# Performance work log

Measured on AMD Instinct MI355X. Metric: run time of the kernel, lower is better.

The kernel has to match this reference:

```python
import jax, jax.numpy as jnp
import numpy as np

B, S, DIM, DA = 64, 4096, 256, 64
NEG = -1e30

def setup_inputs() -> dict:
    key = jax.random.key(0)
    k1, k2, k3, k4 = jax.random.split(key, 4)
    h = jax.random.normal(k1, (B, S, DIM), dtype=jnp.float32)
    mask = jax.random.randint(k2, (B, S), 0, 2).astype(jnp.bool_)
    # xavier_uniform with gain=1.414 as in the torch module
    lim_a = 1.414 * np.sqrt(6.0 / (DIM + DA))
    lim_b = 1.414 * np.sqrt(6.0 / (DA + 1))
    a = jax.random.uniform(k3, (DIM, DA), minval=-lim_a, maxval=lim_a, dtype=jnp.float32)
    b = jax.random.uniform(k4, (DA, 1), minval=-lim_b, maxval=lim_b, dtype=jnp.float32)
    return {"h": h, "mask": mask, "a": a, "b": b}

def reference(h, mask, a, b):
    # e: (B, S) additive-attention logits
    e = jnp.einsum('bsk,ko->bs', jnp.tanh(jnp.einsum('bsd,dk->bsk', h, a)), b)
    e = e + mask.astype(e.dtype) * NEG  # True == padding -> -1e30
    attn = jax.nn.softmax(e, axis=1)    # softmax over seq dim
    # weighted sum over seq: (B, DIM)
    return jnp.einsum('bs,bsd->bd', attn, h)
```

## Files before the change

kernel.cpp:

```cpp
#include <hip/hip_runtime.h>
#include <hip/hip_bf16.h>

#define B_      64
#define S_      4096
#define DIM_    256
#define DA_     64
#define NEG_    (-1e30f)
#define CHUNKS_ 16
#define ROWS_   256
#define TILES_  4
#define LDH_    264
#define PSTR_   258

typedef _Float16 half8 __attribute__((ext_vector_type(8)));
typedef float float4v __attribute__((ext_vector_type(4)));

__global__ __launch_bounds__(256) void prep_kernel(
    const float* __restrict__ a, const void* __restrict__ mask,
    _Float16* __restrict__ at_sw, int* __restrict__ flag)
{
    int idx = blockIdx.x * 256 + threadIdx.x;
    int j    = idx & 7;
    int lane = (idx >> 3) & 63;
    int kbnt = idx >> 9;
    int kb   = kbnt & 7;
    int nt   = kbnt >> 3;
    int d  = kb * 32 + (lane >> 4) * 8 + j;
    int kf = nt * 16 + (lane & 15);
    at_sw[idx] = (_Float16)a[d * DA_ + kf];

    if (blockIdx.x == 0) {
        __shared__ int anynz;
        if (threadIdx.x == 0) anynz = 0;
        __syncthreads();
        const unsigned char* mb = (const unsigned char*)mask;
        int base = threadIdx.x * 4;
        int v = mb[base + 1] | mb[base + 2] | mb[base + 3];
        if (v) atomicOr(&anynz, 1);
        __syncthreads();
        if (threadIdx.x == 0) *flag = (anynz == 0) ? 1 : 0;
    }
}

__global__ __launch_bounds__(256) void fused_kernel(
    const float* __restrict__ h, const _Float16* __restrict__ at_sw,
    const float* __restrict__ bvec, const void* __restrict__ mask,
    const int* __restrict__ flag, float* __restrict__ part)
{
    __shared__ _Float16 hf[64 * LDH_];
    __shared__ float e_l[64];
    __shared__ float w_l[64];
    __shared__ float red[4 * 256];
    __shared__ float m_s, l_s, resc_s;

    const int t = threadIdx.x;
    const int b = blockIdx.x >> 4;
    const int c = blockIdx.x & (CHUNKS_ - 1);
    const int wave = t >> 6;
    const int lane = t & 63;
    const int quad = lane >> 4;
    const int nrow = lane & 15;
    const bool int32enc = (*flag != 0);

    if (t == 0) { m_s = NEG_; l_s = 0.f; }

    const float* hb = h + ((long long)b * S_ + c * ROWS_) * DIM_;
    float bv[4];
    #pragma unroll
    for (int nt = 0; nt < 4; ++nt) bv[nt] = bvec[nt * 16 + nrow];

    const int dbase = (t & 63) * 4;
    float acc0 = 0.f, acc1 = 0.f, acc2 = 0.f, acc3 = 0.f;

    for (int tile = 0; tile < TILES_; ++tile) {
        const float* hsrc = hb + (size_t)tile * 64 * DIM_;
        #pragma unroll
        for (int j = 0; j < 8; ++j) {
            int f2 = t + j * 256;
            int row = f2 >> 5;
            int col = (f2 & 31) * 8;
            const float* src = hsrc + row * DIM_ + col;
            float4 v0 = *(const float4*)(src);
            float4 v1 = *(const float4*)(src + 4);
            union { _Float16 hh[8]; uint4 u; } pk;
            pk.hh[0] = (_Float16)v0.x; pk.hh[1] = (_Float16)v0.y;
            pk.hh[2] = (_Float16)v0.z; pk.hh[3] = (_Float16)v0.w;
            pk.hh[4] = (_Float16)v1.x; pk.hh[5] = (_Float16)v1.y;
            pk.hh[6] = (_Float16)v1.z; pk.hh[7] = (_Float16)v1.w;
            *(uint4*)&hf[row * LDH_ + col] = pk.u;
        }
        __syncthreads();

        float4v accm[4];
        #pragma unroll
        for (int nt = 0; nt < 4; ++nt) accm[nt] = (float4v){0.f, 0.f, 0.f, 0.f};
        const _Float16* hrow = &hf[(wave * 16 + nrow) * LDH_];
        #pragma unroll
        for (int kb = 0; kb < 8; ++kb) {
            half8 af = *(const half8*)(hrow + kb * 32 + quad * 8);
            #pragma unroll
            for (int nt = 0; nt < 4; ++nt) {
                half8 bf = *(const half8*)(at_sw + ((nt * 8 + kb) * 64 + lane) * 8);
                accm[nt] = __builtin_amdgcn_mfma_f32_16x16x32_f16(af, bf, accm[nt], 0, 0, 0);
            }
        }
        #pragma unroll
        for (int r = 0; r < 4; ++r) {
            float p = 0.f;
            #pragma unroll
            for (int nt = 0; nt < 4; ++nt) p += tanhf(accm[nt][r]) * bv[nt];
            p += __shfl_xor(p, 1);
            p += __shfl_xor(p, 2);
            p += __shfl_xor(p, 4);
            p += __shfl_xor(p, 8);
            if (nrow == r) e_l[wave * 16 + quad * 4 + r] = p;
        }
        __syncthreads();

        if (wave == 0) {
            long long mi = (long long)b * S_ + c * ROWS_ + tile * 64 + lane;
            int mv = int32enc ? ((const int*)mask)[mi]
                              : (int)((const unsigned char*)mask)[mi];
            float ev = mv ? NEG_ : e_l[lane];
            float mx = ev;
            #pragma unroll
            for (int off = 32; off >= 1; off >>= 1) mx = fmaxf(mx, __shfl_xor(mx, off));
            float m_old = m_s;
            float m_new = fmaxf(m_old, mx);
            float wv_ = __expf(ev - m_new);
            w_l[lane] = wv_;
            float sm = wv_;
            #pragma unroll
            for (int off = 32; off >= 1; off >>= 1) sm += __shfl_xor(sm, off);
            if (lane == 0) {
                float rs = __expf(m_old - m_new);
                l_s = l_s * rs + sm;
                m_s = m_new;
                resc_s = rs;
            }
        }
        __syncthreads();

        float rs = resc_s;
        acc0 *= rs; acc1 *= rs; acc2 *= rs; acc3 *= rs;
        #pragma unroll 4
        for (int i = 0; i < 16; ++i) {
            int s = i * 4 + wave;
            float ws = w_l[s];
            union { ushort4 u; _Float16 hh[4]; } pk;
            pk.u = *(const ushort4*)((const unsigned short*)&hf[s * LDH_ + dbase]);
            acc0 = fmaf(ws, (float)pk.hh[0], acc0);
            acc1 = fmaf(ws, (float)pk.hh[1], acc1);
            acc2 = fmaf(ws, (float)pk.hh[2], acc2);
            acc3 = fmaf(ws, (float)pk.hh[3], acc3);
        }
        __syncthreads();
    }

    red[wave * 256 + dbase + 0] = acc0;
    red[wave * 256 + dbase + 1] = acc1;
    red[wave * 256 + dbase + 2] = acc2;
    red[wave * 256 + dbase + 3] = acc3;
    __syncthreads();
    float sum = red[t] + red[256 + t] + red[512 + t] + red[768 + t];
    float* pc = part + (size_t)(b * CHUNKS_ + c) * PSTR_;
    pc[2 + t] = sum;
    if (t == 0) { pc[0] = m_s; pc[1] = l_s; }
}

__global__ __launch_bounds__(256) void merge_kernel(
    const float* __restrict__ part, float* __restrict__ out)
{
    const int b = blockIdx.x;
    const int t = threadIdx.x;
    const float* pb = part + (size_t)b * CHUNKS_ * PSTR_;
    float M = NEG_;
    #pragma unroll
    for (int c = 0; c < CHUNKS_; ++c) M = fmaxf(M, pb[c * PSTR_]);
    float L = 0.f, o = 0.f;
    #pragma unroll
    for (int c = 0; c < CHUNKS_; ++c) {
        float sc = __expf(pb[c * PSTR_] - M);
        L += pb[c * PSTR_ + 1] * sc;
        o += pb[c * PSTR_ + 2 + t] * sc;
    }
    out[b * DIM_ + t] = o / L;
}

extern "C" void kernel_launch(void* const* d_in, const int* in_sizes, int n_in,
                              void* d_out, int out_size, void* d_ws, size_t ws_size,
                              hipStream_t stream) {
    const float* h    = (const float*)d_in[0];
    const void*  mask = d_in[1];
    const float* a    = (const float*)d_in[2];
    const float* bvec = (const float*)d_in[3];
    float* out = (float*)d_out;

    char* ws = (char*)d_ws;
    _Float16* at_sw = (_Float16*)ws;
    int* flag       = (int*)(ws + 32768);
    float* part     = (float*)(ws + 36864);

    prep_kernel<<<64, 256, 0, stream>>>(a, mask, at_sw, flag);
    fused_kernel<<<B_ * CHUNKS_, 256, 0, stream>>>(h, at_sw, bvec, mask, flag, part);
    merge_kernel<<<B_, 256, 0, stream>>>(part, out);
}
```

Baseline: 377.0 us.

## Keep h tiles in registers with per-wave online softmax, drop LDS staging

Each wave now loads its own 16 rows of h directly into registers as fp16 MFMA B-operands. The projection matrix is staged once in LDS, and the MFMA operands are swapped. Softmax and the weighted sum are done per wave with a lazily rescaled running max, and the four waves are merged at the end. This removes the per-tile LDS round trip of h and most block-wide barriers, and swaps tanhf for an exp/rcp approximation. The cost is 64 float accumulators per thread, which raises register pressure, plus cross-lane shuffle reductions at the end.

```diff
diff --git a/kernel.cpp b/kernel.cpp
--- a/kernel.cpp
+++ b/kernel.cpp
@@ -8,12 +8,15 @@
 #define NEG_    (-1e30f)
 #define CHUNKS_ 16
 #define ROWS_   256
-#define TILES_  4
-#define LDH_    264
 #define PSTR_   258
 
 typedef _Float16 half8 __attribute__((ext_vector_type(8)));
 typedef float float4v __attribute__((ext_vector_type(4)));
+
+__device__ __forceinline__ float tanh_fast(float x) {
+    float e = __expf(2.0f * x);
+    return 1.0f - 2.0f * __builtin_amdgcn_rcpf(e + 1.0f);
+}
 
 __global__ __launch_bounds__(256) void prep_kernel(
     const float* __restrict__ a, const void* __restrict__ mask,
@@ -42,16 +45,15 @@
     }
 }
 
-__global__ __launch_bounds__(256) void fused_kernel(
+__global__ __launch_bounds__(256, 3) void fused_kernel(
     const float* __restrict__ h, const _Float16* __restrict__ at_sw,
     const float* __restrict__ bvec, const void* __restrict__ mask,
     const int* __restrict__ flag, float* __restrict__ part)
 {
-    __shared__ _Float16 hf[64 * LDH_];
-    __shared__ float e_l[64];
-    __shared__ float w_l[64];
+    __shared__ _Float16 asw[16384];
+    __shared__ float bv_l[64];
     __shared__ float red[4 * 256];
-    __shared__ float m_s, l_s, resc_s;
+    __shared__ float ml[8];
 
     const int t = threadIdx.x;
     const int b = blockIdx.x >> 4;
@@ -62,110 +64,126 @@
     const int nrow = lane & 15;
     const bool int32enc = (*flag != 0);
 
-    if (t == 0) { m_s = NEG_; l_s = 0.f; }
-
-    const float* hb = h + ((long long)b * S_ + c * ROWS_) * DIM_;
-    float bv[4];
-    #pragma unroll
-    for (int nt = 0; nt < 4; ++nt) bv[nt] = bvec[nt * 16 + nrow];
-
-    const int dbase = (t & 63) * 4;
-    float acc0 = 0.f, acc1 = 0.f, acc2 = 0.f, acc3 = 0.f;
-
-    for (int tile = 0; tile < TILES_; ++tile) {
-        const float* hsrc = hb + (size_t)tile * 64 * DIM_;
-        #pragma unroll
-        for (int j = 0; j < 8; ++j) {
-            int f2 = t + j * 256;
-            int row = f2 >> 5;
-            int col = (f2 & 31) * 8;
-            const float* src = hsrc + row * DIM_ + col;
-            float4 v0 = *(const float4*)(src);
-            float4 v1 = *(const float4*)(src + 4);
-            union { _Float16 hh[8]; uint4 u; } pk;
-            pk.hh[0] = (_Float16)v0.x; pk.hh[1] = (_Float16)v0.y;
-            pk.hh[2] = (_Float16)v0.z; pk.hh[3] = (_Float16)v0.w;
-            pk.hh[4] = (_Float16)v1.x; pk.hh[5] = (_Float16)v1.y;
-            pk.hh[6] = (_Float16)v1.z; pk.hh[7] = (_Float16)v1.w;
-            *(uint4*)&hf[row * LDH_ + col] = pk.u;
-        }
-        __syncthreads();
-
-        float4v accm[4];
-        #pragma unroll
-        for (int nt = 0; nt < 4; ++nt) accm[nt] = (float4v){0.f, 0.f, 0.f, 0.f};
-        const _Float16* hrow = &hf[(wave * 16 + nrow) * LDH_];
+    {
+        const uint4* g = (const uint4*)at_sw;
+        uint4* l = (uint4*)asw;
+        #pragma unroll
+        for (int i = 0; i < 8; ++i) l[i * 256 + t] = g[i * 256 + t];
+        if (t < 64) bv_l[t] = bvec[t];
+    }
+    __syncthreads();
+
+    const float* hl = h + (size_t)(b * S_ + c * ROWS_ + wave * 16 + nrow) * DIM_
+                        + quad * 8;
+    const long long mbase = (long long)b * S_ + c * ROWS_ + wave * 16 + nrow;
+
+    float o[64];
+    #pragma unroll
+    for (int i = 0; i < 64; ++i) o[i] = 0.f;
+    float m_w = NEG_, l_w = 0.f;
+
+    #pragma unroll 1
+    for (int round = 0; round < 4; ++round) {
+        const float* hr = hl + (size_t)round * 64 * DIM_;
+
+        half8 hfr[8];
         #pragma unroll
         for (int kb = 0; kb < 8; ++kb) {
-            half8 af = *(const half8*)(hrow + kb * 32 + quad * 8);
+            float4 va = *(const float4*)(hr + kb * 32);
+            float4 vb = *(const float4*)(hr + kb * 32 + 4);
+            union { _Float16 hh[8]; half8 v; } pk;
+            pk.hh[0] = (_Float16)va.x; pk.hh[1] = (_Float16)va.y;
+            pk.hh[2] = (_Float16)va.z; pk.hh[3] = (_Float16)va.w;
+            pk.hh[4] = (_Float16)vb.x; pk.hh[5] = (_Float16)vb.y;
+            pk.hh[6] = (_Float16)vb.z; pk.hh[7] = (_Float16)vb.w;
+            hfr[kb] = pk.v;
+        }
+
+        float4v acc[4];
+        #pragma unroll
+        for (int nt = 0; nt < 4; ++nt) acc[nt] = (float4v){0.f, 0.f, 0.f, 0.f};
+        #pragma unroll
+        for (int kb = 0; kb < 8; ++kb) {
             #pragma unroll
             for (int nt = 0; nt < 4; ++nt) {
-                half8 bf = *(const half8*)(at_sw + ((nt * 8 + kb) * 64 + lane) * 8);
-                accm[nt] = __builtin_amdgcn_mfma_f32_16x16x32_f16(af, bf, accm[nt], 0, 0, 0);
+                half8 af = *(const half8*)&asw[((nt * 8 + kb) * 64 + lane) * 8];
+                acc[nt] = __builtin_amdgcn_mfma_f32_16x16x32_f16(af, hfr[kb], acc[nt], 0, 0, 0);
             }
         }
-        #pragma unroll
-        for (int r = 0; r < 4; ++r) {
-            float p = 0.f;
+
+        float p = 0.f;
+        #pragma unroll
+        for (int nt = 0; nt < 4; ++nt) {
+            float4 bq = *(const float4*)&bv_l[nt * 16 + quad * 4];
+            p += tanh_fast(acc[nt][0]) * bq.x;
+            p += tanh_fast(acc[nt][1]) * bq.y;
+            p += tanh_fast(acc[nt][2]) * bq.z;
+            p += tanh_fast(acc[nt][3]) * bq.w;
+        }
+        p += __shfl_xor(p, 16);
+        p += __shfl_xor(p, 32);
+
+        long long mi = mbase + (long long)round * 64;
+        int mv = int32enc ? ((const int*)mask)[mi]
+                          : (int)((const unsigned char*)mask)[mi];
+        float ev = mv ? NEG_ : p;
+
+        float mx = ev;
+        mx = fmaxf(mx, __shfl_xor(mx, 1));
+        mx = fmaxf(mx, __shfl_xor(mx, 2));
+        mx = fmaxf(mx, __shfl_xor(mx, 4));
+        mx = fmaxf(mx, __shfl_xor(mx, 8));
+        if (mx > m_w + 8.f) {
+            float rs = __expf(m_w - mx);
+            l_w *= rs;
             #pragma unroll
-            for (int nt = 0; nt < 4; ++nt) p += tanhf(accm[nt][r]) * bv[nt];
-            p += __shfl_xor(p, 1);
-            p += __shfl_xor(p, 2);
-            p += __shfl_xor(p, 4);
-            p += __shfl_xor(p, 8);
-            if (nrow == r) e_l[wave * 16 + quad * 4 + r] = p;
-        }
-        __syncthreads();
-
-        if (wave == 0) {
-            long long mi = (long long)b * S_ + c * ROWS_ + tile * 64 + lane;
-            int mv = int32enc ? ((const int*)mask)[mi]
-                              : (int)((const unsigned char*)mask)[mi];
-            float ev = mv ? NEG_ : e_l[lane];
-            float mx = ev;
+            for (int i = 0; i < 64; ++i) o[i] *= rs;
+            m_w = mx;
+        }
+        float w_s = __expf(ev - m_w);
+        float sm = w_s;
+        sm += __shfl_xor(sm, 1);
+        sm += __shfl_xor(sm, 2);
+        sm += __shfl_xor(sm, 4);
+        sm += __shfl_xor(sm, 8);
+        l_w += sm;
+
+        #pragma unroll
+        for (int kb = 0; kb < 8; ++kb) {
             #pragma unroll
-            for (int off = 32; off >= 1; off >>= 1) mx = fmaxf(mx, __shfl_xor(mx, off));
-            float m_old = m_s;
-            float m_new = fmaxf(m_old, mx);
-            float wv_ = __expf(ev - m_new);
-            w_l[lane] = wv_;
-            float sm = wv_;
-            #pragma unroll
-            for (int off = 32; off >= 1; off >>= 1) sm += __shfl_xor(sm, off);
-            if (lane == 0) {
-                float rs = __expf(m_old - m_new);
-                l_s = l_s * rs + sm;
-                m_s = m_new;
-                resc_s = rs;
-            }
-        }
-        __syncthreads();
-
-        float rs = resc_s;
-        acc0 *= rs; acc1 *= rs; acc2 *= rs; acc3 *= rs;
-        #pragma unroll 4
-        for (int i = 0; i < 16; ++i) {
-            int s = i * 4 + wave;
-            float ws = w_l[s];
-            union { ushort4 u; _Float16 hh[4]; } pk;
-            pk.u = *(const ushort4*)((const unsigned short*)&hf[s * LDH_ + dbase]);
-            acc0 = fmaf(ws, (float)pk.hh[0], acc0);
-            acc1 = fmaf(ws, (float)pk.hh[1], acc1);
-            acc2 = fmaf(ws, (float)pk.hh[2], acc2);
-            acc3 = fmaf(ws, (float)pk.hh[3], acc3);
-        }
-        __syncthreads();
-    }
-
-    red[wave * 256 + dbase + 0] = acc0;
-    red[wave * 256 + dbase + 1] = acc1;
-    red[wave * 256 + dbase + 2] = acc2;
-    red[wave * 256 + dbase + 3] = acc3;
+            for (int j = 0; j < 8; ++j)
+                o[kb * 8 + j] = fmaf(w_s, (float)hfr[kb][j], o[kb * 8 + j]);
+        }
+    }
+
+    #pragma unroll
+    for (int i = 0; i < 64; ++i) {
+        o[i] += __shfl_xor(o[i], 1);
+        o[i] += __shfl_xor(o[i], 2);
+        o[i] += __shfl_xor(o[i], 4);
+        o[i] += __shfl_xor(o[i], 8);
+    }
+    #pragma unroll
+    for (int i = 0; i < 64; ++i) {
+        if ((i >> 2) == nrow) {
+            int d = (i >> 3) * 32 + quad * 8 + (i & 7);
+            red[wave * 256 + d] = o[i];
+        }
+    }
+    if (lane == 0) { ml[wave] = m_w; ml[4 + wave] = l_w; }
     __syncthreads();
-    float sum = red[t] + red[256 + t] + red[512 + t] + red[768 + t];
+
+    float M = fmaxf(fmaxf(ml[0], ml[1]), fmaxf(ml[2], ml[3]));
+    float L = 0.f, O = 0.f;
+    #pragma unroll
+    for (int w2 = 0; w2 < 4; ++w2) {
+        float sc = __expf(ml[w2] - M);
+        L += ml[4 + w2] * sc;
+        O = fmaf(red[w2 * 256 + t], sc, O);
+    }
     float* pc = part + (size_t)(b * CHUNKS_ + c) * PSTR_;
-    pc[2 + t] = sum;
-    if (t == 0) { pc[0] = m_s; pc[1] = l_s; }
+    pc[2 + t] = O;
+    if (t == 0) { pc[0] = M; pc[1] = L; }
 }
 
 __global__ __launch_bounds__(256) void merge_kernel(
```

Result: slower. 473.6 us (+25.6%).
